# Kernel tuning notes

Measured on AMD Instinct MI355X. Metric: run time of the kernel, lower is better.

Reference implementation:

```python
import jax, jax.numpy as jnp
import numpy as np

N = 100_000          # nodes
E = 1_600_000        # edges (before self-loops)
D_NODE = 128
D_EDGE = 16
H1, C1 = 8, 8        # conv1: heads=8, out=8 -> concat dim 64
D_EMB = 64           # conv2: heads=1, out=embedding_dim, concat=False
NEG_SLOPE = 0.2      # GATv2 LeakyReLU slope (PyG default)


def _glorot(key, shape, fan):
    return jax.random.normal(key, shape, jnp.float32) * (1.0 / np.sqrt(fan))


def setup_inputs() -> dict:
    key = jax.random.key(0)
    ks = jax.random.split(key, 16)
    return {
        "x": jax.random.normal(ks[0], (N, D_NODE), jnp.float32),
        "edge_index": jax.random.randint(ks[1], (2, E), 0, N, jnp.int64),
        "edge_attr": jax.random.normal(ks[2], (E, D_EDGE), jnp.float32),
        # conv1 params
        "Wl1": _glorot(ks[3], (D_NODE, H1 * C1), D_NODE),
        "bl1": jnp.zeros((H1 * C1,), jnp.float32),
        "Wr1": _glorot(ks[4], (D_NODE, H1 * C1), D_NODE),
        "br1": jnp.zeros((H1 * C1,), jnp.float32),
        "We1": _glorot(ks[5], (D_EDGE, H1 * C1), D_EDGE),
        "att1": _glorot(ks[6], (H1, C1), C1),
        "b1": jnp.zeros((H1 * C1,), jnp.float32),
        # conv2 params (heads=1)
        "Wl2": _glorot(ks[7], (H1 * C1, D_EMB), H1 * C1),
        "bl2": jnp.zeros((D_EMB,), jnp.float32),
        "Wr2": _glorot(ks[8], (H1 * C1, D_EMB), H1 * C1),
        "br2": jnp.zeros((D_EMB,), jnp.float32),
        "We2": _glorot(ks[9], (D_EDGE, D_EMB), D_EDGE),
        "att2": _glorot(ks[10], (1, D_EMB), D_EMB),
        "b2": jnp.zeros((D_EMB,), jnp.float32),
    }


def _add_self_loops(edge_index, edge_attr, n):
    # PyG add_self_loops with fill_value='mean': self-loop edge_attr = mean of
    # incoming edge attrs per destination node.
    src, dst = edge_index[0], edge_index[1]
    ones = jnp.ones((src.shape[0],), edge_attr.dtype)
    deg = jax.ops.segment_sum(ones, dst, num_segments=n)
    ea_mean = jax.ops.segment_sum(edge_attr, dst, num_segments=n)
    ea_mean = ea_mean / jnp.maximum(deg, 1.0)[:, None]
    loop = jnp.arange(n, dtype=src.dtype)
    src2 = jnp.concatenate([src, loop])
    dst2 = jnp.concatenate([dst, loop])
    ea2 = jnp.concatenate([edge_attr, ea_mean], axis=0)
    return src2, dst2, ea2


def _segment_softmax(scores, seg, n):
    # scores: [E, H], seg: [E] destination-node ids
    m = jax.ops.segment_max(scores, seg, num_segments=n)
    m = jnp.where(jnp.isfinite(m), m, 0.0)          # empty segments -> 0
    e = jnp.exp(scores - m[seg])
    s = jax.ops.segment_sum(e, seg, num_segments=n)
    return e / (s[seg] + 1e-16)


def _gatv2(x, src, dst, ea, Wl, bl, Wr, br, We, att, bias, heads, ch, concat):
    n = x.shape[0]
    xl = (x @ Wl + bl).reshape(n, heads, ch)        # W_l x (messages)
    xr = (x @ Wr + br).reshape(n, heads, ch)        # W_r x (queries)
    ee = (ea @ We).reshape(-1, heads, ch)           # edge features
    z = jax.nn.leaky_relu(xl[src] + xr[dst] + ee, NEG_SLOPE)  # [E,H,C]
    score = jnp.einsum('ehc,hc->eh', z, att)
    alpha = _segment_softmax(score, dst, n)         # per-dst softmax
    out = jax.ops.segment_sum(xl[src] * alpha[:, :, None], dst, num_segments=n)
    out = out.reshape(n, heads * ch) if concat else out.mean(axis=1)
    return out + bias


def reference(x, edge_index, edge_attr,
              Wl1, bl1, Wr1, br1, We1, att1, b1,
              Wl2, bl2, Wr2, br2, We2, att2, b2):
    n = x.shape[0]
    src, dst, ea = _add_self_loops(edge_index, edge_attr, n)
    # dropout layers are no-ops in eval mode
    h = jax.nn.elu(_gatv2(x, src, dst, ea, Wl1, bl1, Wr1, br1, We1, att1, b1,
                          H1, C1, True))
    out = _gatv2(h, src, dst, ea, Wl2, bl2, Wr2, br2, We2, att2, b2,
                 1, D_EMB, False)
    return out
```

## Files before the change

### kernel.cpp

```cpp
#include <hip/hip_runtime.h>
#include <hip/hip_bf16.h>

typedef __hip_bfloat16 bf16;

struct Ptrs16 { const void* p[16]; };

__device__ __constant__ int wcnt[14] = {8192,64,8192,64,1024,64,64,4096,64,4096,64,1024,64,64};
__device__ __constant__ int woff[14] = {0,8192,8256,16448,16512,17536,17600,17664,21760,21824,25920,25984,27008,27072};
#define WTOTAL 27136

__global__ void detect_float(Ptrs16 ptrs, int n0, int n1, int* __restrict__ flags)
{
    int b = blockIdx.x, lane = threadIdx.x;
    int count = (b == 0) ? n0 : (b == 1) ? n1 : wcnt[b - 2];
    int limit = count < 1024 ? count : 1024;
    const unsigned short* us = (const unsigned short*)ptrs.p[b];
    int found = 0;
    for (int i = lane; i < limit; i += 64) {
        int e = (us[i] >> 7) & 0xFF;
        if (e >= 143) found = 1;
    }
    unsigned long long any = __ballot(found);
    if (lane == 0) flags[b] = (any != 0ull) ? 0 : 1;
}

__global__ void detect_idx(const int* __restrict__ ei, int* __restrict__ emode)
{
    if (threadIdx.x == 0) {
        int allz = 1;
        for (int i = 0; i < 128; i++)
            if (ei[2 * i + 1] != 0) { allz = 0; break; }
        emode[0] = allz;
    }
}

__global__ __launch_bounds__(256) void convert_weights(
    Ptrs16 ptrs, const int* __restrict__ flags, float* __restrict__ dst)
{
    int i = blockIdx.x * 256 + threadIdx.x;
    if (i >= WTOTAL) return;
    int r = 0;
    while (r < 13 && i >= woff[r + 1]) r++;
    int j = i - woff[r];
    const void* src = ptrs.p[2 + r];
    float v = flags[2 + r] ? __bfloat162float(((const bf16*)src)[j])
                           : ((const float*)src)[j];
    dst[i] = v;
}

__global__ __launch_bounds__(256) void count_kernel(
    const int* __restrict__ ei, int* __restrict__ deg,
    const int* __restrict__ emode, int E, int N)
{
    int e = blockIdx.x * 256 + threadIdx.x;
    if (e >= E) return;
    int stride = 1 + emode[0];
    int d = ei[(E + e) * stride];
    if ((unsigned)d >= (unsigned)N) d = 0;
    atomicAdd(&deg[d], 1);
}

__global__ __launch_bounds__(256) void scan1(
    const int* __restrict__ deg, int* __restrict__ rowptr,
    int* __restrict__ bsum, int N)
{
    __shared__ int ts[256];
    int b = blockIdx.x, t = threadIdx.x;
    int base = b * 1024 + t * 4;
    int v[4]; int s = 0;
#pragma unroll
    for (int i = 0; i < 4; i++) {
        int idx = base + i;
        v[i] = (idx < N) ? deg[idx] : 0;
        s += v[i];
    }
    ts[t] = s;
    __syncthreads();
    for (int off = 1; off < 256; off <<= 1) {
        int x = (t >= off) ? ts[t - off] : 0;
        __syncthreads();
        ts[t] += x;
        __syncthreads();
    }
    int run = (t == 0) ? 0 : ts[t - 1];
#pragma unroll
    for (int i = 0; i < 4; i++) {
        run += v[i];
        int idx = base + i;
        if (idx < N) rowptr[idx + 1] = run;
    }
    if (t == 255) bsum[b] = ts[255];
}

__global__ __launch_bounds__(256) void scan2(int* __restrict__ bsum, int nb)
{
    __shared__ int s[256];
    int t = threadIdx.x;
    s[t] = (t < nb) ? bsum[t] : 0;
    __syncthreads();
    for (int off = 1; off < 256; off <<= 1) {
        int v = (t >= off) ? s[t - off] : 0;
        __syncthreads();
        s[t] += v;
        __syncthreads();
    }
    if (t < nb) bsum[t] = (t == 0) ? 0 : s[t - 1];
}

__global__ __launch_bounds__(256) void scan3(
    int* __restrict__ rowptr, int* __restrict__ fill,
    const int* __restrict__ bsum, int N)
{
    int i = blockIdx.x * 256 + threadIdx.x;
    if (i > N) return;
    int v = (i == 0) ? 0 : rowptr[i] + bsum[(i - 1) >> 10];
    rowptr[i] = v;
    if (i < N) fill[i] = v;
}

__global__ __launch_bounds__(256) void scatter_kernel(
    const int* __restrict__ ei, int* __restrict__ fill,
    int2* __restrict__ edges, const int* __restrict__ emode, int E, int N)
{
    int e = blockIdx.x * 256 + threadIdx.x;
    if (e >= E) return;
    int stride = 1 + emode[0];
    int d = ei[(E + e) * stride];
    int s = ei[e * stride];
    if ((unsigned)d >= (unsigned)N) d = 0;
    if ((unsigned)s >= (unsigned)N) s = 0;
    int pos = atomicAdd(&fill[d], 1);
    edges[pos] = make_int2(s, e);
}

__global__ __launch_bounds__(256) void ea_gather(
    const int2* __restrict__ edges, const float* __restrict__ ea,
    float* __restrict__ ea_csr, int* __restrict__ src_csr, int E)
{
    long base = (long)blockIdx.x * 64;
    int t = threadIdx.x;
    long pos = base + (t >> 2);
    int ch = t & 3;
    if (pos < E) {
        int2 se = edges[pos];
        const float4* ea4 = (const float4*)ea;
        float4 v = ea4[(unsigned)se.y * 4 + ch];
        ((float4*)ea_csr)[pos * 4 + ch] = v;
        if (ch == 0) src_csr[pos] = se.x;
    }
}

template<int K>
__global__ __launch_bounds__(256) void node_gemm(
    const float* __restrict__ X,
    const float* __restrict__ W0, const float* __restrict__ bias0, float* __restrict__ out0,
    const float* __restrict__ W1, const float* __restrict__ bias1, float* __restrict__ out1,
    int N)
{
    const float* W    = blockIdx.y ? W1 : W0;
    const float* bias = blockIdx.y ? bias1 : bias0;
    float* out        = blockIdx.y ? out1 : out0;

    __shared__ float Ws[K * 64];
    __shared__ float xs[4][4][K];

    for (int idx = threadIdx.x; idx < K * 64; idx += 256)
        Ws[idx] = W[idx];

    int wave = threadIdx.x >> 6, lane = threadIdx.x & 63;
    int r0 = blockIdx.x * 16 + wave * 4;
#pragma unroll
    for (int i = 0; i < 4; i++) {
        int r = r0 + i;
        for (int k = lane; k < K; k += 64)
            xs[wave][i][k] = (r < N) ? X[(long)r * K + k] : 0.0f;
    }
    __syncthreads();

    float a0 = 0.f, a1 = 0.f, a2 = 0.f, a3 = 0.f;
#pragma unroll 8
    for (int k = 0; k < K; k++) {
        float w = Ws[k * 64 + lane];
        a0 += xs[wave][0][k] * w;
        a1 += xs[wave][1][k] * w;
        a2 += xs[wave][2][k] * w;
        a3 += xs[wave][3][k] * w;
    }
    float bz = bias[lane];
    if (r0 + 0 < N) out[(long)(r0 + 0) * 64 + lane] = a0 + bz;
    if (r0 + 1 < N) out[(long)(r0 + 1) * 64 + lane] = a1 + bz;
    if (r0 + 2 < N) out[(long)(r0 + 2) * 64 + lane] = a2 + bz;
    if (r0 + 3 < N) out[(long)(r0 + 3) * 64 + lane] = a3 + bz;
}

template<int CPH, bool FINAL>
__global__ __launch_bounds__(256) void edge_kernel(
    const int* __restrict__ rowptr, const int* __restrict__ src_csr,
    const float* __restrict__ ea_csr,
    const float* __restrict__ xl, const float* __restrict__ xr,
    const float* __restrict__ We, const float* __restrict__ att,
    const float* __restrict__ bias, float* __restrict__ outp, int N)
{
    int lane = threadIdx.x & 63;
    int wave = __builtin_amdgcn_readfirstlane(threadIdx.x >> 6);
    int n = blockIdx.x * 4 + wave;
    if (n >= N) return;

    float wcol[16];
#pragma unroll
    for (int k = 0; k < 16; k++) wcol[k] = We[k * 64 + lane];
    float attc = att[lane];
    float xrc  = xr[(unsigned)n * 64 + lane];

    int p0 = rowptr[n], p1 = rowptr[n + 1];
    int deg = p1 - p0;

    float lA = 0.f, accA = 0.f, eeAs = 0.f;
    float lB = 0.f, accB = 0.f, eeBs = 0.f;

    auto body = [&](float4 a0, float4 a1, float4 a2, float4 a3, float xls,
                    float& l, float& acc, float& ees) {
        float t0 = a0.x*wcol[0]  + a0.y*wcol[1];
        float t1 = a0.z*wcol[2]  + a0.w*wcol[3];
        float t2 = a1.x*wcol[4]  + a1.y*wcol[5];
        float t3 = a1.z*wcol[6]  + a1.w*wcol[7];
        float t4 = a2.x*wcol[8]  + a2.y*wcol[9];
        float t5 = a2.z*wcol[10] + a2.w*wcol[11];
        float t6 = a3.x*wcol[12] + a3.y*wcol[13];
        float t7 = a3.z*wcol[14] + a3.w*wcol[15];
        float ee = ((t0 + t1) + (t2 + t3)) + ((t4 + t5) + (t6 + t7));
        ees += ee;
        float z = xls + xrc + ee;
        z = (z > 0.f) ? z : 0.2f * z;
        float t = z * attc;
#pragma unroll
        for (int off = 1; off < CPH; off <<= 1) t += __shfl_xor(t, off, 64);
        float pe = __expf(t);
        l   += pe;
        acc += pe * xls;
    };

    if (deg > 0) {
        const float4* ea4 = (const float4*)ea_csr;
        int pl = p1 - 1;

        int sA = __builtin_amdgcn_readfirstlane(src_csr[p0]);
        int pB = (p0 + 1 < p1) ? p0 + 1 : pl;
        int sB = __builtin_amdgcn_readfirstlane(src_csr[pB]);

        float4 A0 = ea4[(unsigned)p0*4+0], A1 = ea4[(unsigned)p0*4+1],
               A2 = ea4[(unsigned)p0*4+2], A3 = ea4[(unsigned)p0*4+3];
        float  xA = xl[(unsigned)sA*64 + lane];
        float4 B0 = ea4[(unsigned)pB*4+0], B1 = ea4[(unsigned)pB*4+1],
               B2 = ea4[(unsigned)pB*4+2], B3 = ea4[(unsigned)pB*4+3];
        float  xB = xl[(unsigned)sB*64 + lane];

        int p = p0;
        for (; p + 1 < p1; p += 2) {
            float4 c0 = A0, c1 = A1, c2 = A2, c3 = A3; float cx = xA;
            int pa = (p + 2 <= pl) ? p + 2 : pl;
            int sN = __builtin_amdgcn_readfirstlane(src_csr[pa]);
            A0 = ea4[(unsigned)pa*4+0]; A1 = ea4[(unsigned)pa*4+1];
            A2 = ea4[(unsigned)pa*4+2]; A3 = ea4[(unsigned)pa*4+3];
            xA = xl[(unsigned)sN*64 + lane];
            body(c0, c1, c2, c3, cx, lA, accA, eeAs);

            float4 d0 = B0, d1 = B1, d2 = B2, d3 = B3; float dx = xB;
            int pb = (p + 3 <= pl) ? p + 3 : pl;
            int sM = __builtin_amdgcn_readfirstlane(src_csr[pb]);
            B0 = ea4[(unsigned)pb*4+0]; B1 = ea4[(unsigned)pb*4+1];
            B2 = ea4[(unsigned)pb*4+2]; B3 = ea4[(unsigned)pb*4+3];
            xB = xl[(unsigned)sM*64 + lane];
            body(d0, d1, d2, d3, dx, lB, accB, eeBs);
        }
        if (p < p1)
            body(A0, A1, A2, A3, xA, lA, accA, eeAs);
    }

    float l = lA + lB, acc = accA + accB, eeacc = eeAs + eeBs;

    {
        float eeS = (deg > 0) ? eeacc / (float)deg : 0.f;
        float xls = xl[(unsigned)n * 64 + lane];
        float z = xls + xrc + eeS;
        z = (z > 0.f) ? z : 0.2f * z;
        float t = z * attc;
#pragma unroll
        for (int off = 1; off < CPH; off <<= 1) t += __shfl_xor(t, off, 64);
        float pe = __expf(t);
        l   += pe;
        acc += pe * xls;
    }

    float out = acc / (l + 1e-16f);
    float v = out + bias[lane];
    if (FINAL) {
        outp[(unsigned)n * 64 + lane] = v;
    } else {
        outp[(unsigned)n * 64 + lane] = (v > 0.f) ? v : (__expf(v) - 1.f);
    }
}

extern "C" void kernel_launch(void* const* d_in, const int* in_sizes, int n_in,
                              void* d_out, int out_size, void* d_ws, size_t ws_size,
                              hipStream_t stream)
{
    const int N = in_sizes[0] / 128;
    const int E = (in_sizes[1] >= 6000000) ? in_sizes[1] / 4 : in_sizes[1] / 2;

    const int*   ei = (const int*)  d_in[1];
    const float* x  = (const float*)d_in[0];
    const float* ea = (const float*)d_in[2];

    Ptrs16 ptrs;
    ptrs.p[0] = d_in[0];
    ptrs.p[1] = d_in[2];
    for (int i = 0; i < 14; i++) ptrs.p[2 + i] = d_in[3 + i];

    char* p = (char*)d_ws;
    auto carve = [&](size_t bytes) {
        char* r = p;
        p += (bytes + 255) & ~(size_t)255;
        return r;
    };
    int*   flags   = (int*)  carve(256);
    int*   emode   = (int*)  carve(256);
    float* wts     = (float*)carve((size_t)WTOTAL * 4);
    int*   deg     = (int*)  carve((size_t)N * 4);
    int*   rowptr  = (int*)  carve((size_t)(N + 1) * 4);
    int*   fill    = (int*)  carve((size_t)N * 4);
    int2*  edges   = (int2*) carve((size_t)E * 8);
    int*   bsum    = (int*)  carve(1024);
    float* xl      = (float*)carve((size_t)N * 64 * 4);
    float* xr      = (float*)carve((size_t)N * 64 * 4);
    float* h       = (float*)carve((size_t)N * 64 * 4);
    float* ea_csr  = (float*)carve((size_t)E * 16 * 4);
    int*   src_csr = (int*)  carve((size_t)E * 4);
    (void)ws_size; (void)n_in; (void)out_size;

    const float* Wl1f  = wts + 0;     const float* bl1f = wts + 8192;
    const float* Wr1f  = wts + 8256;  const float* br1f = wts + 16448;
    const float* We1f  = wts + 16512; const float* att1f= wts + 17536;
    const float* b1f   = wts + 17600;
    const float* Wl2f  = wts + 17664; const float* bl2f = wts + 21760;
    const float* Wr2f  = wts + 21824; const float* br2f = wts + 25920;
    const float* We2f  = wts + 25984; const float* att2f= wts + 27008;
    const float* b2f   = wts + 27072;

    hipMemsetAsync(deg, 0, (size_t)N * 4, stream);

    detect_float<<<16, 64, 0, stream>>>(ptrs, in_sizes[0], in_sizes[2], flags);
    detect_idx<<<1, 64, 0, stream>>>(ei, emode);
    convert_weights<<<(WTOTAL + 255) / 256, 256, 0, stream>>>(ptrs, flags, wts);

    count_kernel<<<(E + 255) / 256, 256, 0, stream>>>(ei, deg, emode, E, N);

    int nb = (N + 1023) / 1024;
    scan1<<<nb, 256, 0, stream>>>(deg, rowptr, bsum, N);
    scan2<<<1, 256, 0, stream>>>(bsum, nb);
    scan3<<<(N + 256) / 256, 256, 0, stream>>>(rowptr, fill, bsum, N);

    scatter_kernel<<<(E + 255) / 256, 256, 0, stream>>>(ei, fill, edges, emode, E, N);

    ea_gather<<<(E + 63) / 64, 256, 0, stream>>>(edges, ea, ea_csr, src_csr, E);

    dim3 g1((N + 15) / 16, 2);
    node_gemm<128><<<g1, 256, 0, stream>>>(x, Wl1f, bl1f, xl, Wr1f, br1f, xr, N);
    int ng = (N + 3) / 4;
    edge_kernel<8, false><<<ng, 256, 0, stream>>>(
        rowptr, src_csr, ea_csr, xl, xr, We1f, att1f, b1f, h, N);

    node_gemm<64><<<g1, 256, 0, stream>>>(h, Wl2f, bl2f, xl, Wr2f, br2f, xr, N);
    edge_kernel<64, true><<<ng, 256, 0, stream>>>(
        rowptr, src_csr, ea_csr, xl, xr, We2f, att2f, b2f, (float*)d_out, N);
}
```

Baseline: 997.2 us.

## Fuse edge scatter with attribute gather and stage edge features through LDS

The scatter kernel now writes source ids and the 64-byte edge-attribute rows straight into CSR order. This removes the intermediate int2 edge array and the separate ea_gather launch and its extra pass over memory, at the cost of scattered 64-byte writes. The edge kernel loads edge attributes for 16 edges per wave as one coalesced float4-per-lane read into shared memory, prefetching the next chunk. It also keeps four xl gathers in flight instead of two. Buffers are padded by 16 edges so the chunked loads can read past the end safely.

```diff
diff --git a/kernel.cpp b/kernel.cpp
--- a/kernel.cpp
+++ b/kernel.cpp
@@ -120,7 +120,8 @@
 
 __global__ __launch_bounds__(256) void scatter_kernel(
     const int* __restrict__ ei, int* __restrict__ fill,
-    int2* __restrict__ edges, const int* __restrict__ emode, int E, int N)
+    const float* __restrict__ ea, float* __restrict__ ea_csr,
+    int* __restrict__ src_csr, const int* __restrict__ emode, int E, int N)
 {
     int e = blockIdx.x * 256 + threadIdx.x;
     if (e >= E) return;
@@ -129,25 +130,15 @@
     int s = ei[e * stride];
     if ((unsigned)d >= (unsigned)N) d = 0;
     if ((unsigned)s >= (unsigned)N) s = 0;
+    const float4* ea4 = (const float4*)ea;
+    float4 v0 = ea4[(long)e * 4 + 0];
+    float4 v1 = ea4[(long)e * 4 + 1];
+    float4 v2 = ea4[(long)e * 4 + 2];
+    float4 v3 = ea4[(long)e * 4 + 3];
     int pos = atomicAdd(&fill[d], 1);
-    edges[pos] = make_int2(s, e);
-}
-
-__global__ __launch_bounds__(256) void ea_gather(
-    const int2* __restrict__ edges, const float* __restrict__ ea,
-    float* __restrict__ ea_csr, int* __restrict__ src_csr, int E)
-{
-    long base = (long)blockIdx.x * 64;
-    int t = threadIdx.x;
-    long pos = base + (t >> 2);
-    int ch = t & 3;
-    if (pos < E) {
-        int2 se = edges[pos];
-        const float4* ea4 = (const float4*)ea;
-        float4 v = ea4[(unsigned)se.y * 4 + ch];
-        ((float4*)ea_csr)[pos * 4 + ch] = v;
-        if (ch == 0) src_csr[pos] = se.x;
-    }
+    src_csr[pos] = s;
+    float4* dst = (float4*)ea_csr + (long)pos * 4;
+    dst[0] = v0; dst[1] = v1; dst[2] = v2; dst[3] = v3;
 }
 
 template<int K>
@@ -201,6 +192,8 @@
     const float* __restrict__ We, const float* __restrict__ att,
     const float* __restrict__ bias, float* __restrict__ outp, int N)
 {
+    __shared__ float elds[4][256];
+
     int lane = threadIdx.x & 63;
     int wave = __builtin_amdgcn_readfirstlane(threadIdx.x >> 6);
     int n = blockIdx.x * 4 + wave;
@@ -212,72 +205,77 @@
     float attc = att[lane];
     float xrc  = xr[(unsigned)n * 64 + lane];
 
-    int p0 = rowptr[n], p1 = rowptr[n + 1];
+    int p0 = __builtin_amdgcn_readfirstlane(rowptr[n]);
+    int p1 = __builtin_amdgcn_readfirstlane(rowptr[n + 1]);
     int deg = p1 - p0;
 
-    float lA = 0.f, accA = 0.f, eeAs = 0.f;
-    float lB = 0.f, accB = 0.f, eeBs = 0.f;
-
-    auto body = [&](float4 a0, float4 a1, float4 a2, float4 a3, float xls,
-                    float& l, float& acc, float& ees) {
-        float t0 = a0.x*wcol[0]  + a0.y*wcol[1];
-        float t1 = a0.z*wcol[2]  + a0.w*wcol[3];
-        float t2 = a1.x*wcol[4]  + a1.y*wcol[5];
-        float t3 = a1.z*wcol[6]  + a1.w*wcol[7];
-        float t4 = a2.x*wcol[8]  + a2.y*wcol[9];
-        float t5 = a2.z*wcol[10] + a2.w*wcol[11];
-        float t6 = a3.x*wcol[12] + a3.y*wcol[13];
-        float t7 = a3.z*wcol[14] + a3.w*wcol[15];
-        float ee = ((t0 + t1) + (t2 + t3)) + ((t4 + t5) + (t6 + t7));
-        ees += ee;
-        float z = xls + xrc + ee;
-        z = (z > 0.f) ? z : 0.2f * z;
-        float t = z * attc;
-#pragma unroll
-        for (int off = 1; off < CPH; off <<= 1) t += __shfl_xor(t, off, 64);
-        float pe = __expf(t);
-        l   += pe;
-        acc += pe * xls;
-    };
+    float l0 = 0.f, acc0 = 0.f, ees0 = 0.f;
+    float l1 = 0.f, acc1 = 0.f, ees1 = 0.f;
+
+#define BODY(I, XS, LL, AC, EE_) do {                                        \
+    if (cbase + (I) < p1) {                                                  \
+        const float4* ep_ = (const float4*)(lb + (I) * 16);                  \
+        float4 a0 = ep_[0], a1 = ep_[1], a2 = ep_[2], a3 = ep_[3];           \
+        float xls = XS;                                                      \
+        int pn_ = cbase + (I) + 4; pn_ = (pn_ <= pl) ? pn_ : pl;             \
+        int sn_ = __builtin_amdgcn_readfirstlane(src_csr[pn_]);              \
+        XS = xl[(unsigned)sn_ * 64 + lane];                                  \
+        float t0 = a0.x*wcol[0]  + a0.y*wcol[1];                             \
+        float t1 = a0.z*wcol[2]  + a0.w*wcol[3];                             \
+        float t2 = a1.x*wcol[4]  + a1.y*wcol[5];                             \
+        float t3 = a1.z*wcol[6]  + a1.w*wcol[7];                             \
+        float t4 = a2.x*wcol[8]  + a2.y*wcol[9];                             \
+        float t5 = a2.z*wcol[10] + a2.w*wcol[11];                            \
+        float t6 = a3.x*wcol[12] + a3.y*wcol[13];                            \
+        float t7 = a3.z*wcol[14] + a3.w*wcol[15];                            \
+        float ee = ((t0 + t1) + (t2 + t3)) + ((t4 + t5) + (t6 + t7));        \
+        EE_ += ee;                                                           \
+        float z = xls + xrc + ee;                                            \
+        z = (z > 0.f) ? z : 0.2f * z;                                        \
+        float t = z * attc;                                                  \
+        _Pragma("unroll")                                                    \
+        for (int off_ = 1; off_ < CPH; off_ <<= 1)                           \
+            t += __shfl_xor(t, off_, 64);                                    \
+        float pe = __expf(t);                                                \
+        LL += pe; AC += pe * xls;                                            \
+    } } while (0)
 
     if (deg > 0) {
-        const float4* ea4 = (const float4*)ea_csr;
+        const float4* ea4c = (const float4*)ea_csr;
+        float* lb = &elds[wave][0];
         int pl = p1 - 1;
 
+        float4 nxt = ea4c[(long)p0 * 4 + lane];
+        int iB = (p0 + 1 <= pl) ? p0 + 1 : pl;
+        int iC = (p0 + 2 <= pl) ? p0 + 2 : pl;
+        int iD = (p0 + 3 <= pl) ? p0 + 3 : pl;
         int sA = __builtin_amdgcn_readfirstlane(src_csr[p0]);
-        int pB = (p0 + 1 < p1) ? p0 + 1 : pl;
-        int sB = __builtin_amdgcn_readfirstlane(src_csr[pB]);
-
-        float4 A0 = ea4[(unsigned)p0*4+0], A1 = ea4[(unsigned)p0*4+1],
-               A2 = ea4[(unsigned)p0*4+2], A3 = ea4[(unsigned)p0*4+3];
-        float  xA = xl[(unsigned)sA*64 + lane];
-        float4 B0 = ea4[(unsigned)pB*4+0], B1 = ea4[(unsigned)pB*4+1],
-               B2 = ea4[(unsigned)pB*4+2], B3 = ea4[(unsigned)pB*4+3];
-        float  xB = xl[(unsigned)sB*64 + lane];
-
-        int p = p0;
-        for (; p + 1 < p1; p += 2) {
-            float4 c0 = A0, c1 = A1, c2 = A2, c3 = A3; float cx = xA;
-            int pa = (p + 2 <= pl) ? p + 2 : pl;
-            int sN = __builtin_amdgcn_readfirstlane(src_csr[pa]);
-            A0 = ea4[(unsigned)pa*4+0]; A1 = ea4[(unsigned)pa*4+1];
-            A2 = ea4[(unsigned)pa*4+2]; A3 = ea4[(unsigned)pa*4+3];
-            xA = xl[(unsigned)sN*64 + lane];
-            body(c0, c1, c2, c3, cx, lA, accA, eeAs);
-
-            float4 d0 = B0, d1 = B1, d2 = B2, d3 = B3; float dx = xB;
-            int pb = (p + 3 <= pl) ? p + 3 : pl;
-            int sM = __builtin_amdgcn_readfirstlane(src_csr[pb]);
-            B0 = ea4[(unsigned)pb*4+0]; B1 = ea4[(unsigned)pb*4+1];
-            B2 = ea4[(unsigned)pb*4+2]; B3 = ea4[(unsigned)pb*4+3];
-            xB = xl[(unsigned)sM*64 + lane];
-            body(d0, d1, d2, d3, dx, lB, accB, eeBs);
+        int sB = __builtin_amdgcn_readfirstlane(src_csr[iB]);
+        int sC = __builtin_amdgcn_readfirstlane(src_csr[iC]);
+        int sD = __builtin_amdgcn_readfirstlane(src_csr[iD]);
+        float x0 = xl[(unsigned)sA * 64 + lane];
+        float x1 = xl[(unsigned)sB * 64 + lane];
+        float x2 = xl[(unsigned)sC * 64 + lane];
+        float x3 = xl[(unsigned)sD * 64 + lane];
+
+        int nch = (deg + 15) >> 4;
+        for (int ch = 0; ch < nch; ch++) {
+            int cbase = p0 + (ch << 4);
+            ((float4*)lb)[lane] = nxt;
+            if (ch + 1 < nch)
+                nxt = ea4c[(long)(cbase + 16) * 4 + lane];
+#pragma unroll
+            for (int g = 0; g < 4; g++) {
+                BODY(g * 4 + 0, x0, l0, acc0, ees0);
+                BODY(g * 4 + 1, x1, l1, acc1, ees1);
+                BODY(g * 4 + 2, x2, l0, acc0, ees0);
+                BODY(g * 4 + 3, x3, l1, acc1, ees1);
+            }
         }
-        if (p < p1)
-            body(A0, A1, A2, A3, xA, lA, accA, eeAs);
-    }
-
-    float l = lA + lB, acc = accA + accB, eeacc = eeAs + eeBs;
+    }
+#undef BODY
+
+    float l = l0 + l1, acc = acc0 + acc1, eeacc = ees0 + ees1;
 
     {
         float eeS = (deg > 0) ? eeacc / (float)deg : 0.f;
@@ -329,13 +327,12 @@
     int*   deg     = (int*)  carve((size_t)N * 4);
     int*   rowptr  = (int*)  carve((size_t)(N + 1) * 4);
     int*   fill    = (int*)  carve((size_t)N * 4);
-    int2*  edges   = (int2*) carve((size_t)E * 8);
     int*   bsum    = (int*)  carve(1024);
     float* xl      = (float*)carve((size_t)N * 64 * 4);
     float* xr      = (float*)carve((size_t)N * 64 * 4);
     float* h       = (float*)carve((size_t)N * 64 * 4);
-    float* ea_csr  = (float*)carve((size_t)E * 16 * 4);
-    int*   src_csr = (int*)  carve((size_t)E * 4);
+    float* ea_csr  = (float*)carve((size_t)(E + 16) * 16 * 4);
+    int*   src_csr = (int*)  carve((size_t)(E + 16) * 4);
     (void)ws_size; (void)n_in; (void)out_size;
 
     const float* Wl1f  = wts + 0;     const float* bl1f = wts + 8192;
@@ -360,9 +357,8 @@
     scan2<<<1, 256, 0, stream>>>(bsum, nb);
     scan3<<<(N + 256) / 256, 256, 0, stream>>>(rowptr, fill, bsum, N);
 
-    scatter_kernel<<<(E + 255) / 256, 256, 0, stream>>>(ei, fill, edges, emode, E, N);
-
-    ea_gather<<<(E + 63) / 64, 256, 0, stream>>>(edges, ea, ea_csr, src_csr, E);
+    scatter_kernel<<<(E + 255) / 256, 256, 0, stream>>>(
+        ei, fill, ea, ea_csr, src_csr, emode, E, N);
 
     dim3 g1((N + 15) / 16, 2);
     node_gemm<128><<<g1, 256, 0, stream>>>(x, Wl1f, bl1f, xl, Wr1f, br1f, xr, N);
```

Result: faster. 858.8 us (-13.9%).
